# Kernel tuning notes

Measured on AMD Instinct MI355X. Metric: run time of the kernel, lower is better.

Reference implementation:

```python
import jax, jax.numpy as jnp
import numpy as np

VOCAB, EMB, HID, CTXD = 32000, 512, 1024, 2048
B, T, L = 64, 64, 64

def setup_inputs() -> dict:
    key = jax.random.key(0)
    ks = jax.random.split(key, 10)
    return {
        "tgt": jax.random.randint(ks[0], (B, T), 0, VOCAB, dtype=jnp.int64 if jax.config.jax_enable_x64 else jnp.int32),
        "ctx": jax.random.normal(ks[1], (B, L, CTXD), dtype=jnp.float32),
        "h0": jax.random.normal(ks[2], (B, HID), dtype=jnp.float32),
        "ctx_lengths": jax.random.randint(ks[3], (B,), 1, L + 1),
        "emb_table": jax.random.normal(ks[4], (VOCAB, EMB), dtype=jnp.float32) * 0.01,
        "W_a": jax.random.normal(ks[5], (HID, CTXD), dtype=jnp.float32) * 0.01,
        "W_ih": jax.random.normal(ks[6], (3 * HID, EMB + CTXD), dtype=jnp.float32) * 0.01,
        "W_hh": jax.random.normal(ks[7], (3 * HID, HID), dtype=jnp.float32) * 0.01,
        "b_ih": jnp.zeros((3 * HID,), dtype=jnp.float32),
        "b_hh": jnp.zeros((3 * HID,), dtype=jnp.float32),
    }

def reference(tgt, ctx, h0, ctx_lengths, emb_table, W_a, W_ih, W_hh, b_ih, b_hh):
    H = h0.shape[-1]
    Lc = ctx.shape[1]
    # length mask over context positions: [B, L]
    mask = jnp.arange(Lc)[None, :] < ctx_lengths[:, None]
    # precompute 'general' attention projection of ctx: [B, L, H]
    ctxW = jnp.einsum('blc,hc->blh', ctx, W_a)
    emb = emb_table[tgt]  # [B, T, E]

    def step(h, e_t):
        # Bahdanau-style: attend with previous hidden state
        scores = jnp.einsum('bh,blh->bl', h, ctxW)
        scores = jnp.where(mask, scores, jnp.float32(-1e9))
        attn = jax.nn.softmax(scores, axis=-1)
        c_t = jnp.einsum('bl,blc->bc', attn, ctx)  # [B, CTXD]
        x = jnp.concatenate([e_t, c_t], axis=-1)   # [B, E+CTXD]
        gx = x @ W_ih.T + b_ih                      # [B, 3H]
        gh = h @ W_hh.T + b_hh                      # [B, 3H]
        r = jax.nn.sigmoid(gx[:, :H] + gh[:, :H])
        z = jax.nn.sigmoid(gx[:, H:2 * H] + gh[:, H:2 * H])
        n = jnp.tanh(gx[:, 2 * H:] + r * gh[:, 2 * H:])
        h_new = (1.0 - z) * n + z * h
        return h_new, h_new

    h_last, outs = jax.lax.scan(step, h0, jnp.swapaxes(emb, 0, 1))
    return jnp.swapaxes(outs, 0, 1), h_last  # (B, T, H), (B, H)
```

## Files before the change

kernel.cpp:

```cpp
#include <hip/hip_runtime.h>
#include <hip/hip_bf16.h>


using short8 = __attribute__((ext_vector_type(8))) short;
using f32x4  = __attribute__((ext_vector_type(4))) float;

#define FLAG_ACC 1
#define FLAG_BF  2

__device__ __forceinline__ void gld16(const void* g, void* l) {
  __builtin_amdgcn_global_load_lds(
      (const __attribute__((address_space(1))) unsigned int*)g,
      (__attribute__((address_space(3))) unsigned int*)l, 16, 0, 0);
}


__global__ __launch_bounds__(256) void split_bf16_kernel(
    const float* __restrict__ x, __hip_bfloat16* __restrict__ hi,
    __hip_bfloat16* __restrict__ lo, int n)
{
  int i = blockIdx.x * blockDim.x + threadIdx.x;
  int stride = gridDim.x * blockDim.x;
  for (; i < n; i += stride) {
    float v = x[i];
    __hip_bfloat16 h = __float2bfloat16(v);
    hi[i] = h;
    lo[i] = __float2bfloat16(v - __bfloat162float(h));
  }
}

__global__ __launch_bounds__(256) void prep_weights(
    const float* __restrict__ Wih, const float* __restrict__ Whh,
    const float* __restrict__ bih, const float* __restrict__ bhh,
    __hip_bfloat16* __restrict__ WcH, __hip_bfloat16* __restrict__ WcL,
    __hip_bfloat16* __restrict__ We,
    __hip_bfloat16* __restrict__ WhH, __hip_bfloat16* __restrict__ WhL,
    float* __restrict__ bihp, float* __restrict__ bhhp)
{
  const int jp = blockIdx.x;
  const int u = jp / 3, g = jp - 3 * u;
  const int src = g * 1024 + u;
  for (int c = threadIdx.x; c < 2048; c += 256) {
    float v = Wih[(size_t)src * 2560 + 512 + c];
    __hip_bfloat16 h = __float2bfloat16(v);
    WcH[(size_t)jp * 2048 + c] = h;
    WcL[(size_t)jp * 2048 + c] = __float2bfloat16(v - __bfloat162float(h));
  }
  for (int c = threadIdx.x; c < 512; c += 256)
    We[(size_t)jp * 512 + c] = __float2bfloat16(Wih[(size_t)src * 2560 + c]);
  for (int c = threadIdx.x; c < 1024; c += 256) {
    float v = Whh[(size_t)src * 1024 + c];
    __hip_bfloat16 h = __float2bfloat16(v);
    WhH[(size_t)jp * 1024 + c] = h;
    WhL[(size_t)jp * 1024 + c] = __float2bfloat16(v - __bfloat162float(h));
  }
  if (threadIdx.x == 0) { bihp[jp] = bih[src]; bhhp[jp] = bhh[src]; }
}

__global__ __launch_bounds__(256) void emb_gather(
    const int* __restrict__ tgt, const float* __restrict__ table,
    __hip_bfloat16* __restrict__ outb)
{
  const int row = blockIdx.x;
  const int v = tgt[row];
  for (int c = threadIdx.x; c < 512; c += 256)
    outb[(size_t)row * 512 + c] = __float2bfloat16(table[(size_t)v * 512 + c]);
}

__global__ __launch_bounds__(256) void h0_init(
    const float* __restrict__ h0, float* __restrict__ hf,
    __hip_bfloat16* __restrict__ hhi, __hip_bfloat16* __restrict__ hlo)
{
  const int i = blockIdx.x * 256 + threadIdx.x;
  float v = h0[i];
  hf[i] = v;
  __hip_bfloat16 h = __float2bfloat16(v);
  hhi[i] = h;
  hlo[i] = __float2bfloat16(v - __bfloat162float(h));
}


__global__ __launch_bounds__(256) void gemm_bt(
    const short* __restrict__ A, const short* __restrict__ B,
    float* __restrict__ Cf, __hip_bfloat16* __restrict__ Cb,
    const float* __restrict__ bias, int M, int N, int K, int flags)
{
  __shared__ __align__(16) short As[128 * 32];
  __shared__ __align__(16) short Bs[128 * 32];
  const int tid = threadIdx.x, lane = tid & 63, w = tid >> 6;
  const int m0 = blockIdx.y * 128, n0 = blockIdx.x * 128;
  const int wm = (w >> 1) * 64, wn = (w & 1) * 64;
  const int srow = lane >> 2, scol = (lane & 3) * 8;
  f32x4 zero = {0.f, 0.f, 0.f, 0.f};
  f32x4 acc[4][4];
#pragma unroll
  for (int i = 0; i < 4; ++i)
#pragma unroll
    for (int j = 0; j < 4; ++j) acc[i][j] = zero;

  for (int k0 = 0; k0 < K; k0 += 32) {
    __syncthreads();
#pragma unroll
    for (int s = 0; s < 2; ++s) {
      const int chunk = w * 2 + s;
      const int r = chunk * 16 + srow;
      gld16(A + (size_t)(m0 + r) * K + k0 + scol, As + chunk * 512);
      gld16(B + (size_t)(n0 + r) * K + k0 + scol, Bs + chunk * 512);
    }
    __syncthreads();
    const int fm = lane & 15, fq = lane >> 4;
    short8 af[4], bq[4];
#pragma unroll
    for (int i = 0; i < 4; ++i)
      af[i] = *(const short8*)(As + (wm + i * 16 + fm) * 32 + fq * 8);
#pragma unroll
    for (int j = 0; j < 4; ++j)
      bq[j] = *(const short8*)(Bs + (wn + j * 16 + fm) * 32 + fq * 8);
#pragma unroll
    for (int i = 0; i < 4; ++i)
#pragma unroll
      for (int j = 0; j < 4; ++j)
        acc[i][j] = __builtin_amdgcn_mfma_f32_16x16x32_bf16(af[i], bq[j], acc[i][j], 0, 0, 0);
  }

  const int cn = lane & 15, cq = (lane >> 4) * 4;
#pragma unroll
  for (int i = 0; i < 4; ++i)
#pragma unroll
    for (int j = 0; j < 4; ++j)
#pragma unroll
      for (int r = 0; r < 4; ++r) {
        const int m = m0 + wm + i * 16 + cq + r;
        const int n = n0 + wn + j * 16 + cn;
        float v = acc[i][j][r];
        if (flags & FLAG_ACC) v += Cf[(size_t)m * N + n];
        if (bias) v += bias[n];
        if (flags & FLAG_BF) Cb[(size_t)m * N + n] = __float2bfloat16(v);
        else                 Cf[(size_t)m * N + n] = v;
      }
}


__global__ __launch_bounds__(256) void gemm_bt3(
    const short* __restrict__ AH, const short* __restrict__ AL,
    const short* __restrict__ BH, const short* __restrict__ BL,
    float* __restrict__ Cf, int M, int N, int K)
{
  __shared__ __align__(16) short AsH[128 * 32];
  __shared__ __align__(16) short AsL[128 * 32];
  __shared__ __align__(16) short BsH[128 * 32];
  __shared__ __align__(16) short BsL[128 * 32];
  const int tid = threadIdx.x, lane = tid & 63, w = tid >> 6;
  const int m0 = blockIdx.y * 128, n0 = blockIdx.x * 128;
  const int wm = (w >> 1) * 64, wn = (w & 1) * 64;
  const int srow = lane >> 2, scol = (lane & 3) * 8;
  f32x4 zero = {0.f, 0.f, 0.f, 0.f};
  f32x4 acc[4][4];
#pragma unroll
  for (int i = 0; i < 4; ++i)
#pragma unroll
    for (int j = 0; j < 4; ++j) acc[i][j] = zero;

  for (int k0 = 0; k0 < K; k0 += 32) {
    __syncthreads();
#pragma unroll
    for (int s = 0; s < 2; ++s) {
      const int chunk = w * 2 + s;
      const int r = chunk * 16 + srow;
      const size_t ao = (size_t)(m0 + r) * K + k0 + scol;
      const size_t bo = (size_t)(n0 + r) * K + k0 + scol;
      gld16(AH + ao, AsH + chunk * 512);
      gld16(AL + ao, AsL + chunk * 512);
      gld16(BH + bo, BsH + chunk * 512);
      gld16(BL + bo, BsL + chunk * 512);
    }
    __syncthreads();
    const int fm = lane & 15, fq = lane >> 4;
    short8 ah[4], al[4], bh[4], bl[4];
#pragma unroll
    for (int i = 0; i < 4; ++i) {
      const int off = (wm + i * 16 + fm) * 32 + fq * 8;
      ah[i] = *(const short8*)(AsH + off);
      al[i] = *(const short8*)(AsL + off);
    }
#pragma unroll
    for (int j = 0; j < 4; ++j) {
      const int off = (wn + j * 16 + fm) * 32 + fq * 8;
      bh[j] = *(const short8*)(BsH + off);
      bl[j] = *(const short8*)(BsL + off);
    }
#pragma unroll
    for (int i = 0; i < 4; ++i)
#pragma unroll
      for (int j = 0; j < 4; ++j) {
        acc[i][j] = __builtin_amdgcn_mfma_f32_16x16x32_bf16(ah[i], bh[j], acc[i][j], 0, 0, 0);
        acc[i][j] = __builtin_amdgcn_mfma_f32_16x16x32_bf16(al[i], bh[j], acc[i][j], 0, 0, 0);
        acc[i][j] = __builtin_amdgcn_mfma_f32_16x16x32_bf16(ah[i], bl[j], acc[i][j], 0, 0, 0);
      }
  }

  const int cn = lane & 15, cq = (lane >> 4) * 4;
#pragma unroll
  for (int i = 0; i < 4; ++i)
#pragma unroll
    for (int j = 0; j < 4; ++j)
#pragma unroll
      for (int r = 0; r < 4; ++r) {
        const int m = m0 + wm + i * 16 + cq + r;
        const int n = n0 + wn + j * 16 + cn;
        Cf[(size_t)m * N + n] = acc[i][j][r];
      }
}


__global__ __launch_bounds__(256) void step_a(
    const float* __restrict__ hf, const float* __restrict__ ctxW,
    const int* __restrict__ lens, float* __restrict__ attn,
    const short* __restrict__ hhi, const short* __restrict__ hlo,
    const short* __restrict__ WhH, const short* __restrict__ WhL,
    float* __restrict__ ghG)
{
  const int tid = threadIdx.x;
  if (blockIdx.x < 64) {
    __shared__ float hs[1024];
    __shared__ float part[256];
    const int b = blockIdx.x;
    const int len = lens[b];
    ((float4*)hs)[tid] = ((const float4*)(hf + b * 1024))[tid];
    __syncthreads();
    const int l = tid >> 2, q = tid & 3;
    float sx = 0.f, sy = 0.f, sz = 0.f, sw = 0.f;
    if (l < len) {
      const float4* row = (const float4*)(ctxW + ((size_t)(b * 64 + l)) * 1024 + q * 256);
      const float4* hh = (const float4*)(hs + q * 256);
#pragma unroll 8
      for (int i = 0; i < 64; ++i) {
        float4 a = row[i], c = hh[i];
        sx += a.x * c.x; sy += a.y * c.y; sz += a.z * c.z; sw += a.w * c.w;
      }
    }
    part[tid] = (sx + sy) + (sz + sw);
    __syncthreads();
    if (tid < 64) {
      float sc = part[tid * 4] + part[tid * 4 + 1] + part[tid * 4 + 2] + part[tid * 4 + 3];
      if (tid >= len) sc = -1e9f;
      float m = sc;
#pragma unroll
      for (int off = 32; off > 0; off >>= 1) m = fmaxf(m, __shfl_xor(m, off));
      float e = __expf(sc - m);
      float sum = e;
#pragma unroll
      for (int off = 32; off > 0; off >>= 1) sum += __shfl_xor(sum, off);
      attn[b * 64 + tid] = e / sum;
    }
  } else {
    const int j0 = (blockIdx.x - 64) * 16;
    const int lane = tid & 63, w = tid >> 6;
    const int fm = lane & 15, fq = lane >> 4;
    f32x4 acc = {0.f, 0.f, 0.f, 0.f};
    const short* ah = hhi + (w * 16 + fm) * 1024 + fq * 8;
    const short* al = hlo + (w * 16 + fm) * 1024 + fq * 8;
    const short* bh = WhH + (size_t)(j0 + fm) * 1024 + fq * 8;
    const short* bl = WhL + (size_t)(j0 + fm) * 1024 + fq * 8;
#pragma unroll 4
    for (int k0 = 0; k0 < 1024; k0 += 32) {
      short8 aH = *(const short8*)(ah + k0);
      short8 aL = *(const short8*)(al + k0);
      short8 b0 = *(const short8*)(bh + k0);
      short8 c0 = *(const short8*)(bl + k0);
      acc = __builtin_amdgcn_mfma_f32_16x16x32_bf16(aH, b0, acc, 0, 0, 0);
      acc = __builtin_amdgcn_mfma_f32_16x16x32_bf16(aL, b0, acc, 0, 0, 0);
      acc = __builtin_amdgcn_mfma_f32_16x16x32_bf16(aH, c0, acc, 0, 0, 0);
    }
    const int mb = w * 16 + fq * 4;
    *(f32x4*)(ghG + (size_t)(j0 + fm) * 64 + mb) = acc;
  }
}


__global__ __launch_bounds__(512) void gate_kernel(
    const float* __restrict__ attn, const int* __restrict__ lens,
    const float* __restrict__ ghG, const float* __restrict__ ctxWc,
    const __hip_bfloat16* __restrict__ gxe, const float* __restrict__ bhhp,
    float* __restrict__ hf, short* __restrict__ hhi, short* __restrict__ hlo,
    float* __restrict__ out, int t)
{
  const int jc = blockIdx.x & 63, bc = blockIdx.x >> 6;
  const int j0 = jc * 48, b0 = bc * 16;
  __shared__ float ghs[48 * 17];
  __shared__ float wv[16][64];
  __shared__ short lidx[16][64];
  __shared__ int   cnt[16];
  __shared__ float ps0[256], ps1[256], ps2[256];
  const int tid = threadIdx.x;
  if (tid < 16) cnt[tid] = 0;
  for (int i = tid; i < 768; i += 512) {
    const int row = i >> 4, col = i & 15;
    ghs[row * 17 + col] = ghG[(size_t)(j0 + row) * 64 + b0 + col];
  }
  __syncthreads();
  if (tid < 256) {
    const int bb = tid >> 4, l4 = (tid & 15) * 4;
    const int b = b0 + bb, len = lens[b];
#pragma unroll
    for (int k = 0; k < 4; ++k) {
      const int l = l4 + k;
      const float wl = attn[b * 64 + l];
      if (l < len && wl >= 1e-8f) {
        const int pos = atomicAdd(&cnt[bb], 1);
        lidx[bb][pos] = (short)l;
        wv[bb][pos] = wl;
      }
    }
  }
  __syncthreads();

  const int tl = tid & 255;
  const int bb = tl >> 4, jg = tl & 15;
  const int b = b0 + bb;
  const int n = cnt[bb];
  const int nh = n >> 1;
  const int ibeg = (tid < 256) ? 0 : nh;
  const int iend = (tid < 256) ? nh : n;
  float g0 = 0.f, g1 = 0.f, g2 = 0.f;
  const float* base = ctxWc + (size_t)(b * 64) * 3072 + j0 + jg * 3;
  int i = ibeg;
  for (; i + 3 < iend; i += 4) {
    const float w0 = wv[bb][i],     w1 = wv[bb][i + 1];
    const float w2 = wv[bb][i + 2], w3 = wv[bb][i + 3];
    const float* p0 = base + (size_t)lidx[bb][i] * 3072;
    const float* p1 = base + (size_t)lidx[bb][i + 1] * 3072;
    const float* p2 = base + (size_t)lidx[bb][i + 2] * 3072;
    const float* p3 = base + (size_t)lidx[bb][i + 3] * 3072;
    const float a0 = __builtin_nontemporal_load(p0);
    const float a1 = __builtin_nontemporal_load(p0 + 1);
    const float a2 = __builtin_nontemporal_load(p0 + 2);
    const float b0v = __builtin_nontemporal_load(p1);
    const float b1v = __builtin_nontemporal_load(p1 + 1);
    const float b2v = __builtin_nontemporal_load(p1 + 2);
    const float c0 = __builtin_nontemporal_load(p2);
    const float c1 = __builtin_nontemporal_load(p2 + 1);
    const float c2 = __builtin_nontemporal_load(p2 + 2);
    const float d0 = __builtin_nontemporal_load(p3);
    const float d1 = __builtin_nontemporal_load(p3 + 1);
    const float d2 = __builtin_nontemporal_load(p3 + 2);
    g0 += (w0 * a0 + w1 * b0v) + (w2 * c0 + w3 * d0);
    g1 += (w0 * a1 + w1 * b1v) + (w2 * c1 + w3 * d1);
    g2 += (w0 * a2 + w1 * b2v) + (w2 * c2 + w3 * d2);
  }
  for (; i < iend; ++i) {
    const float wa = wv[bb][i];
    const float* pa = base + (size_t)lidx[bb][i] * 3072;
    g0 += wa * __builtin_nontemporal_load(pa);
    g1 += wa * __builtin_nontemporal_load(pa + 1);
    g2 += wa * __builtin_nontemporal_load(pa + 2);
  }
  if (tid >= 256) { ps0[tl] = g0; ps1[tl] = g1; ps2[tl] = g2; }
  __syncthreads();
  if (tid < 256) {
    g0 += ps0[tl]; g1 += ps1[tl]; g2 += ps2[tl];

    const int jp = j0 + jg * 3;
    const __hip_bfloat16* ge = gxe + (size_t)(b * 64 + t) * 3072 + jp;
    const float gxr = g0 + __bfloat162float(ge[0]);
    const float gxz = g1 + __bfloat162float(ge[1]);
    const float gxn = g2 + __bfloat162float(ge[2]);
    const float ghr = ghs[(jg * 3 + 0) * 17 + bb] + bhhp[jp + 0];
    const float ghz = ghs[(jg * 3 + 1) * 17 + bb] + bhhp[jp + 1];
    const float ghn = ghs[(jg * 3 + 2) * 17 + bb] + bhhp[jp + 2];
    const float rr = 1.f / (1.f + __expf(-(gxr + ghr)));
    const float zz = 1.f / (1.f + __expf(-(gxz + ghz)));
    const float nn = tanhf(gxn + rr * ghn);
    const int u = jc * 16 + jg;
    const float hold = hf[b * 1024 + u];
    const float hn = (1.f - zz) * nn + zz * hold;
    out[(size_t)(b * 64 + t) * 1024 + u] = hn;
    hf[b * 1024 + u] = hn;
    __hip_bfloat16 hh = __float2bfloat16(hn);
    hhi[b * 1024 + u] = *reinterpret_cast<short*>(&hh);
    __hip_bfloat16 hl = __float2bfloat16(hn - __bfloat162float(hh));
    hlo[b * 1024 + u] = *reinterpret_cast<short*>(&hl);
    if (t == 63) out[(size_t)64 * 64 * 1024 + b * 1024 + u] = hn;
  }
}


extern "C" void kernel_launch(void* const* d_in, const int* in_sizes, int n_in,
                              void* d_out, int out_size, void* d_ws, size_t ws_size,
                              hipStream_t stream)
{
  const int*   tgt  = (const int*)  d_in[0];
  const float* ctx  = (const float*)d_in[1];
  const float* h0   = (const float*)d_in[2];
  const int*   lens = (const int*)  d_in[3];
  const float* embt = (const float*)d_in[4];
  const float* Wa   = (const float*)d_in[5];
  const float* Wih  = (const float*)d_in[6];
  const float* Whh  = (const float*)d_in[7];
  const float* bih  = (const float*)d_in[8];
  const float* bhh  = (const float*)d_in[9];
  float* out = (float*)d_out;

  char* p = (char*)d_ws;
  auto take = [&](size_t bytes) {
    char* q = p;
    p += (bytes + 255) & ~(size_t)255;
    return q;
  };
  short* ctx_hi = (short*)take((size_t)8388608 * 2);
  short* ctx_lo = (short*)take((size_t)8388608 * 2);
  short* Wa_hi  = (short*)take((size_t)2097152 * 2);
  short* Wa_lo  = (short*)take((size_t)2097152 * 2);
  short* WcH    = (short*)take((size_t)3072 * 2048 * 2);
  short* WcL    = (short*)take((size_t)3072 * 2048 * 2);
  short* We_p   = (short*)take((size_t)3072 * 512 * 2);
  short* WhH    = (short*)take((size_t)3072 * 1024 * 2);
  short* WhL    = (short*)take((size_t)3072 * 1024 * 2);
  float* bih_p  = (float*)take(3072 * 4);
  float* bhh_p  = (float*)take(3072 * 4);
  short* emb_bf = (short*)take((size_t)4096 * 512 * 2);
  float* ctxW   = (float*)take((size_t)4096 * 1024 * 4);
  float* ctxWc  = (float*)take((size_t)4096 * 3072 * 4);
  short* gxe    = (short*)take((size_t)4096 * 3072 * 2);
  float* hf     = (float*)take((size_t)65536 * 4);
  short* hhi    = (short*)take((size_t)65536 * 2);
  short* hlo    = (short*)take((size_t)65536 * 2);
  float* attn   = (float*)take((size_t)4096 * 4);
  float* ghG    = (float*)take((size_t)3072 * 64 * 4);

  split_bf16_kernel<<<2048, 256, 0, stream>>>(ctx, (__hip_bfloat16*)ctx_hi,
                                              (__hip_bfloat16*)ctx_lo, 8388608);
  split_bf16_kernel<<<1024, 256, 0, stream>>>(Wa, (__hip_bfloat16*)Wa_hi,
                                              (__hip_bfloat16*)Wa_lo, 2097152);
  prep_weights<<<3072, 256, 0, stream>>>(Wih, Whh, bih, bhh,
      (__hip_bfloat16*)WcH, (__hip_bfloat16*)WcL, (__hip_bfloat16*)We_p,
      (__hip_bfloat16*)WhH, (__hip_bfloat16*)WhL, bih_p, bhh_p);
  emb_gather<<<4096, 256, 0, stream>>>(tgt, embt, (__hip_bfloat16*)emb_bf);
  h0_init<<<256, 256, 0, stream>>>(h0, hf, (__hip_bfloat16*)hhi,
                                   (__hip_bfloat16*)hlo);

  gemm_bt3<<<dim3(8, 32), 256, 0, stream>>>(ctx_hi, ctx_lo, Wa_hi, Wa_lo,
                                            ctxW, 4096, 1024, 2048);
  gemm_bt3<<<dim3(24, 32), 256, 0, stream>>>(ctx_hi, ctx_lo, WcH, WcL,
                                             ctxWc, 4096, 3072, 2048);
  gemm_bt<<<dim3(24, 32), 256, 0, stream>>>(emb_bf, We_p, nullptr,
                                            (__hip_bfloat16*)gxe, bih_p,
                                            4096, 3072, 512, FLAG_BF);

  for (int t = 0; t < 64; ++t) {
    step_a<<<256, 256, 0, stream>>>(hf, ctxW, lens, attn,
                                    hhi, hlo, WhH, WhL, ghG);
    gate_kernel<<<256, 512, 0, stream>>>(attn, lens, ghG, ctxWc,
        (const __hip_bfloat16*)gxe, bhh_p, hf, hhi, hlo, out, t);
  }
}
```

Before: 2.414 ms.

## Fuse per-step recurrence kernels into one persistent cooperative kernel with grid barriers

Replaces the 128 per-timestep launches (step_a and gate_kernel) with a single cooperative persistent kernel of 256 blocks. The blocks synchronise through atomic counter barriers in global memory, and each block reloads h and converts it to hi/lo bf16 in LDS. The Whh GEMM is also split across two K-halves per block, with the halves reduced in shared memory. This targets launch overhead on the serial recurrence, but adds spin-wait barrier cost and relies on relaxed atomics to make writes visible across blocks.

```diff
diff --git a/kernel.cpp b/kernel.cpp
--- a/kernel.cpp
+++ b/kernel.cpp
@@ -7,6 +7,9 @@
 
 #define FLAG_ACC 1
 #define FLAG_BF  2
+
+#define AL(p)    __hip_atomic_load((p), __ATOMIC_RELAXED, __HIP_MEMORY_SCOPE_AGENT)
+#define AS(p, v) __hip_atomic_store((p), (v), __ATOMIC_RELAXED, __HIP_MEMORY_SCOPE_AGENT)
 
 __device__ __forceinline__ void gld16(const void* g, void* l) {
   __builtin_amdgcn_global_load_lds(
@@ -69,14 +72,11 @@
 
 __global__ __launch_bounds__(256) void h0_init(
     const float* __restrict__ h0, float* __restrict__ hf,
-    __hip_bfloat16* __restrict__ hhi, __hip_bfloat16* __restrict__ hlo)
+    unsigned int* __restrict__ bar)
 {
   const int i = blockIdx.x * 256 + threadIdx.x;
-  float v = h0[i];
-  hf[i] = v;
-  __hip_bfloat16 h = __float2bfloat16(v);
-  hhi[i] = h;
-  hlo[i] = __float2bfloat16(v - __bfloat162float(h));
+  hf[i] = h0[i];
+  if (blockIdx.x == 0 && threadIdx.x < 256) bar[threadIdx.x] = 0u;
 }
 
 
@@ -213,174 +213,215 @@
 }
 
 
-__global__ __launch_bounds__(256) void step_a(
-    const float* __restrict__ hf, const float* __restrict__ ctxW,
-    const int* __restrict__ lens, float* __restrict__ attn,
-    const short* __restrict__ hhi, const short* __restrict__ hlo,
+__global__ __launch_bounds__(512, 1) void recurrence_kernel(
+    const float* __restrict__ ctxW, const int* __restrict__ lens,
     const short* __restrict__ WhH, const short* __restrict__ WhL,
-    float* __restrict__ ghG)
-{
+    const float* __restrict__ ctxWc, const __hip_bfloat16* __restrict__ gxe,
+    const float* __restrict__ bhhp, float* __restrict__ hf,
+    float* __restrict__ attn, float* __restrict__ ghG,
+    unsigned int* __restrict__ bar, float* __restrict__ out)
+{
+  const int blk = blockIdx.x;
   const int tid = threadIdx.x;
-  if (blockIdx.x < 64) {
-    __shared__ float hs[1024];
-    __shared__ float part[256];
-    const int b = blockIdx.x;
-    const int len = lens[b];
-    ((float4*)hs)[tid] = ((const float4*)(hf + b * 1024))[tid];
-    __syncthreads();
-    const int l = tid >> 2, q = tid & 3;
-    float sx = 0.f, sy = 0.f, sz = 0.f, sw = 0.f;
-    if (l < len) {
-      const float4* row = (const float4*)(ctxW + ((size_t)(b * 64 + l)) * 1024 + q * 256);
-      const float4* hh = (const float4*)(hs + q * 256);
-#pragma unroll 8
-      for (int i = 0; i < 64; ++i) {
-        float4 a = row[i], c = hh[i];
-        sx += a.x * c.x; sy += a.y * c.y; sz += a.z * c.z; sw += a.w * c.w;
-      }
-    }
-    part[tid] = (sx + sy) + (sz + sw);
-    __syncthreads();
-    if (tid < 64) {
-      float sc = part[tid * 4] + part[tid * 4 + 1] + part[tid * 4 + 2] + part[tid * 4 + 3];
-      if (tid >= len) sc = -1e9f;
-      float m = sc;
-#pragma unroll
-      for (int off = 32; off > 0; off >>= 1) m = fmaxf(m, __shfl_xor(m, off));
-      float e = __expf(sc - m);
-      float sum = e;
-#pragma unroll
-      for (int off = 32; off > 0; off >>= 1) sum += __shfl_xor(sum, off);
-      attn[b * 64 + tid] = e / sum;
-    }
-  } else {
-    const int j0 = (blockIdx.x - 64) * 16;
-    const int lane = tid & 63, w = tid >> 6;
-    const int fm = lane & 15, fq = lane >> 4;
-    f32x4 acc = {0.f, 0.f, 0.f, 0.f};
-    const short* ah = hhi + (w * 16 + fm) * 1024 + fq * 8;
-    const short* al = hlo + (w * 16 + fm) * 1024 + fq * 8;
-    const short* bh = WhH + (size_t)(j0 + fm) * 1024 + fq * 8;
-    const short* bl = WhL + (size_t)(j0 + fm) * 1024 + fq * 8;
-#pragma unroll 4
-    for (int k0 = 0; k0 < 1024; k0 += 32) {
-      short8 aH = *(const short8*)(ah + k0);
-      short8 aL = *(const short8*)(al + k0);
-      short8 b0 = *(const short8*)(bh + k0);
-      short8 c0 = *(const short8*)(bl + k0);
-      acc = __builtin_amdgcn_mfma_f32_16x16x32_bf16(aH, b0, acc, 0, 0, 0);
-      acc = __builtin_amdgcn_mfma_f32_16x16x32_bf16(aL, b0, acc, 0, 0, 0);
-      acc = __builtin_amdgcn_mfma_f32_16x16x32_bf16(aH, c0, acc, 0, 0, 0);
-    }
-    const int mb = w * 16 + fq * 4;
-    *(f32x4*)(ghG + (size_t)(j0 + fm) * 64 + mb) = acc;
-  }
-}
-
-
-__global__ __launch_bounds__(512) void gate_kernel(
-    const float* __restrict__ attn, const int* __restrict__ lens,
-    const float* __restrict__ ghG, const float* __restrict__ ctxWc,
-    const __hip_bfloat16* __restrict__ gxe, const float* __restrict__ bhhp,
-    float* __restrict__ hf, short* __restrict__ hhi, short* __restrict__ hlo,
-    float* __restrict__ out, int t)
-{
-  const int jc = blockIdx.x & 63, bc = blockIdx.x >> 6;
-  const int j0 = jc * 48, b0 = bc * 16;
+
+  __shared__ float hs[1024];
+  __shared__ float part[256];
+  __shared__ __align__(16) short AsH[16 * 1032];
+  __shared__ __align__(16) short AsL[16 * 1032];
+  __shared__ f32x4 psk[4][64];
   __shared__ float ghs[48 * 17];
   __shared__ float wv[16][64];
   __shared__ short lidx[16][64];
   __shared__ int   cnt[16];
   __shared__ float ps0[256], ps1[256], ps2[256];
-  const int tid = threadIdx.x;
-  if (tid < 16) cnt[tid] = 0;
-  for (int i = tid; i < 768; i += 512) {
-    const int row = i >> 4, col = i & 15;
-    ghs[row * 17 + col] = ghG[(size_t)(j0 + row) * 64 + b0 + col];
-  }
-  __syncthreads();
-  if (tid < 256) {
-    const int bb = tid >> 4, l4 = (tid & 15) * 4;
-    const int b = b0 + bb, len = lens[b];
-#pragma unroll
-    for (int k = 0; k < 4; ++k) {
-      const int l = l4 + k;
-      const float wl = attn[b * 64 + l];
-      if (l < len && wl >= 1e-8f) {
-        const int pos = atomicAdd(&cnt[bb], 1);
-        lidx[bb][pos] = (short)l;
-        wv[bb][pos] = wl;
-      }
-    }
-  }
-  __syncthreads();
-
-  const int tl = tid & 255;
-  const int bb = tl >> 4, jg = tl & 15;
-  const int b = b0 + bb;
-  const int n = cnt[bb];
-  const int nh = n >> 1;
-  const int ibeg = (tid < 256) ? 0 : nh;
-  const int iend = (tid < 256) ? nh : n;
-  float g0 = 0.f, g1 = 0.f, g2 = 0.f;
-  const float* base = ctxWc + (size_t)(b * 64) * 3072 + j0 + jg * 3;
-  int i = ibeg;
-  for (; i + 3 < iend; i += 4) {
-    const float w0 = wv[bb][i],     w1 = wv[bb][i + 1];
-    const float w2 = wv[bb][i + 2], w3 = wv[bb][i + 3];
-    const float* p0 = base + (size_t)lidx[bb][i] * 3072;
-    const float* p1 = base + (size_t)lidx[bb][i + 1] * 3072;
-    const float* p2 = base + (size_t)lidx[bb][i + 2] * 3072;
-    const float* p3 = base + (size_t)lidx[bb][i + 3] * 3072;
-    const float a0 = __builtin_nontemporal_load(p0);
-    const float a1 = __builtin_nontemporal_load(p0 + 1);
-    const float a2 = __builtin_nontemporal_load(p0 + 2);
-    const float b0v = __builtin_nontemporal_load(p1);
-    const float b1v = __builtin_nontemporal_load(p1 + 1);
-    const float b2v = __builtin_nontemporal_load(p1 + 2);
-    const float c0 = __builtin_nontemporal_load(p2);
-    const float c1 = __builtin_nontemporal_load(p2 + 1);
-    const float c2 = __builtin_nontemporal_load(p2 + 2);
-    const float d0 = __builtin_nontemporal_load(p3);
-    const float d1 = __builtin_nontemporal_load(p3 + 1);
-    const float d2 = __builtin_nontemporal_load(p3 + 2);
-    g0 += (w0 * a0 + w1 * b0v) + (w2 * c0 + w3 * d0);
-    g1 += (w0 * a1 + w1 * b1v) + (w2 * c1 + w3 * d1);
-    g2 += (w0 * a2 + w1 * b2v) + (w2 * c2 + w3 * d2);
-  }
-  for (; i < iend; ++i) {
-    const float wa = wv[bb][i];
-    const float* pa = base + (size_t)lidx[bb][i] * 3072;
-    g0 += wa * __builtin_nontemporal_load(pa);
-    g1 += wa * __builtin_nontemporal_load(pa + 1);
-    g2 += wa * __builtin_nontemporal_load(pa + 2);
-  }
-  if (tid >= 256) { ps0[tl] = g0; ps1[tl] = g1; ps2[tl] = g2; }
-  __syncthreads();
-  if (tid < 256) {
-    g0 += ps0[tl]; g1 += ps1[tl]; g2 += ps2[tl];
-
-    const int jp = j0 + jg * 3;
-    const __hip_bfloat16* ge = gxe + (size_t)(b * 64 + t) * 3072 + jp;
-    const float gxr = g0 + __bfloat162float(ge[0]);
-    const float gxz = g1 + __bfloat162float(ge[1]);
-    const float gxn = g2 + __bfloat162float(ge[2]);
-    const float ghr = ghs[(jg * 3 + 0) * 17 + bb] + bhhp[jp + 0];
-    const float ghz = ghs[(jg * 3 + 1) * 17 + bb] + bhhp[jp + 1];
-    const float ghn = ghs[(jg * 3 + 2) * 17 + bb] + bhhp[jp + 2];
-    const float rr = 1.f / (1.f + __expf(-(gxr + ghr)));
-    const float zz = 1.f / (1.f + __expf(-(gxz + ghz)));
-    const float nn = tanhf(gxn + rr * ghn);
-    const int u = jc * 16 + jg;
-    const float hold = hf[b * 1024 + u];
-    const float hn = (1.f - zz) * nn + zz * hold;
-    out[(size_t)(b * 64 + t) * 1024 + u] = hn;
-    hf[b * 1024 + u] = hn;
-    __hip_bfloat16 hh = __float2bfloat16(hn);
-    hhi[b * 1024 + u] = *reinterpret_cast<short*>(&hh);
-    __hip_bfloat16 hl = __float2bfloat16(hn - __bfloat162float(hh));
-    hlo[b * 1024 + u] = *reinterpret_cast<short*>(&hl);
-    if (t == 63) out[(size_t)64 * 64 * 1024 + b * 1024 + u] = hn;
+
+  const int g = blk - 64;
+  const int xcd = g & 7, s = g >> 3;
+  const int jc2 = xcd * 6 + (s >> 2);
+  const int bc2 = s & 3;
+
+  for (int t = 0; t < 64; ++t) {
+    if (blk < 64) {
+      const int b = blk;
+      const int len = lens[b];
+      for (int i = tid; i < 1024; i += 512)
+        hs[i] = AL(hf + b * 1024 + i);
+      __syncthreads();
+      if (tid < 256) {
+        const int l = tid >> 2, q = tid & 3;
+        float sx = 0.f, sy = 0.f, sz = 0.f, sw = 0.f;
+        if (l < len) {
+          const float4* row = (const float4*)(ctxW + ((size_t)(b * 64 + l)) * 1024 + q * 256);
+          const float4* hh = (const float4*)(hs + q * 256);
+#pragma unroll 8
+          for (int i = 0; i < 64; ++i) {
+            float4 a = row[i], c = hh[i];
+            sx += a.x * c.x; sy += a.y * c.y; sz += a.z * c.z; sw += a.w * c.w;
+          }
+        }
+        part[tid] = (sx + sy) + (sz + sw);
+      }
+      __syncthreads();
+      if (tid < 64) {
+        float sc = part[tid * 4] + part[tid * 4 + 1] + part[tid * 4 + 2] + part[tid * 4 + 3];
+        if (tid >= len) sc = -1e9f;
+        float m = sc;
+#pragma unroll
+        for (int off = 32; off > 0; off >>= 1) m = fmaxf(m, __shfl_xor(m, off));
+        float e = __expf(sc - m);
+        float sum = e;
+#pragma unroll
+        for (int off = 32; off > 0; off >>= 1) sum += __shfl_xor(sum, off);
+        AS(attn + b * 64 + tid, e / sum);
+      }
+    } else {
+      for (int i = tid; i < 16384; i += 512) {
+        const int row = i >> 10, col = i & 1023;
+        float v = AL(hf + (bc2 * 16 + row) * 1024 + col);
+        __hip_bfloat16 hh = __float2bfloat16(v);
+        AsH[row * 1032 + col] = *reinterpret_cast<short*>(&hh);
+        __hip_bfloat16 hl = __float2bfloat16(v - __bfloat162float(hh));
+        AsL[row * 1032 + col] = *reinterpret_cast<short*>(&hl);
+      }
+      __syncthreads();
+      const int lane = tid & 63, w = tid >> 6;
+      const int fm = lane & 15, fq = lane >> 4;
+      const int jsub = w & 3, khalf = w >> 2;
+      const int jr = jc2 * 64 + jsub * 16 + fm;
+      const short* bh = WhH + (size_t)jr * 1024 + fq * 8;
+      const short* bl = WhL + (size_t)jr * 1024 + fq * 8;
+      const short* arH = AsH + fm * 1032 + fq * 8;
+      const short* arL = AsL + fm * 1032 + fq * 8;
+      f32x4 acc = {0.f, 0.f, 0.f, 0.f};
+      const int kbeg = khalf * 512;
+#pragma unroll 4
+      for (int k = kbeg; k < kbeg + 512; k += 32) {
+        short8 aH = *(const short8*)(arH + k);
+        short8 aL = *(const short8*)(arL + k);
+        short8 b0 = *(const short8*)(bh + k);
+        short8 c0 = *(const short8*)(bl + k);
+        acc = __builtin_amdgcn_mfma_f32_16x16x32_bf16(aH, b0, acc, 0, 0, 0);
+        acc = __builtin_amdgcn_mfma_f32_16x16x32_bf16(aL, b0, acc, 0, 0, 0);
+        acc = __builtin_amdgcn_mfma_f32_16x16x32_bf16(aH, c0, acc, 0, 0, 0);
+      }
+      if (khalf) psk[jsub][lane] = acc;
+      __syncthreads();
+      if (!khalf) {
+        f32x4 o = psk[jsub][lane];
+        acc.x += o.x; acc.y += o.y; acc.z += o.z; acc.w += o.w;
+        const size_t bidx = (size_t)jr * 64 + bc2 * 16 + fq * 4;
+        AS(ghG + bidx + 0, acc.x);
+        AS(ghG + bidx + 1, acc.y);
+        AS(ghG + bidx + 2, acc.z);
+        AS(ghG + bidx + 3, acc.w);
+      }
+    }
+
+    __syncthreads();
+    if (tid == 0) {
+      __hip_atomic_fetch_add(&bar[t * 2], 1u, __ATOMIC_RELAXED, __HIP_MEMORY_SCOPE_AGENT);
+      while (AL(&bar[t * 2]) < 256u) __builtin_amdgcn_s_sleep(2);
+    }
+    __syncthreads();
+
+    {
+      const int jc = blk & 63, bc = blk >> 6;
+      const int j0 = jc * 48, b0 = bc * 16;
+      if (tid < 16) cnt[tid] = 0;
+      for (int i = tid; i < 768; i += 512) {
+        const int row = i >> 4, col = i & 15;
+        ghs[row * 17 + col] = AL(ghG + (size_t)(j0 + row) * 64 + b0 + col);
+      }
+      __syncthreads();
+      if (tid < 256) {
+        const int bb = tid >> 4, l4 = (tid & 15) * 4;
+        const int b = b0 + bb, len = lens[b];
+#pragma unroll
+        for (int k = 0; k < 4; ++k) {
+          const int l = l4 + k;
+          const float wl = AL(attn + b * 64 + l);
+          if (l < len && wl >= 1e-8f) {
+            const int pos = atomicAdd(&cnt[bb], 1);
+            lidx[bb][pos] = (short)l;
+            wv[bb][pos] = wl;
+          }
+        }
+      }
+      __syncthreads();
+
+      const int tl = tid & 255;
+      const int bb = tl >> 4, jg = tl & 15;
+      const int b = b0 + bb;
+      const int n = cnt[bb];
+      const int nh = n >> 1;
+      const int ibeg = (tid < 256) ? 0 : nh;
+      const int iend = (tid < 256) ? nh : n;
+      float g0 = 0.f, g1 = 0.f, g2 = 0.f;
+      const float* base = ctxWc + (size_t)(b * 64) * 3072 + j0 + jg * 3;
+      int i = ibeg;
+      for (; i + 3 < iend; i += 4) {
+        const float w0 = wv[bb][i],     w1 = wv[bb][i + 1];
+        const float w2 = wv[bb][i + 2], w3 = wv[bb][i + 3];
+        const float* p0 = base + (size_t)lidx[bb][i] * 3072;
+        const float* p1 = base + (size_t)lidx[bb][i + 1] * 3072;
+        const float* p2 = base + (size_t)lidx[bb][i + 2] * 3072;
+        const float* p3 = base + (size_t)lidx[bb][i + 3] * 3072;
+        const float a0 = __builtin_nontemporal_load(p0);
+        const float a1 = __builtin_nontemporal_load(p0 + 1);
+        const float a2 = __builtin_nontemporal_load(p0 + 2);
+        const float b0v = __builtin_nontemporal_load(p1);
+        const float b1v = __builtin_nontemporal_load(p1 + 1);
+        const float b2v = __builtin_nontemporal_load(p1 + 2);
+        const float c0 = __builtin_nontemporal_load(p2);
+        const float c1 = __builtin_nontemporal_load(p2 + 1);
+        const float c2 = __builtin_nontemporal_load(p2 + 2);
+        const float d0 = __builtin_nontemporal_load(p3);
+        const float d1 = __builtin_nontemporal_load(p3 + 1);
+        const float d2 = __builtin_nontemporal_load(p3 + 2);
+        g0 += (w0 * a0 + w1 * b0v) + (w2 * c0 + w3 * d0);
+        g1 += (w0 * a1 + w1 * b1v) + (w2 * c1 + w3 * d1);
+        g2 += (w0 * a2 + w1 * b2v) + (w2 * c2 + w3 * d2);
+      }
+      for (; i < iend; ++i) {
+        const float wa = wv[bb][i];
+        const float* pa = base + (size_t)lidx[bb][i] * 3072;
+        g0 += wa * __builtin_nontemporal_load(pa);
+        g1 += wa * __builtin_nontemporal_load(pa + 1);
+        g2 += wa * __builtin_nontemporal_load(pa + 2);
+      }
+      if (tid >= 256) { ps0[tl] = g0; ps1[tl] = g1; ps2[tl] = g2; }
+      __syncthreads();
+      if (tid < 256) {
+        g0 += ps0[tl]; g1 += ps1[tl]; g2 += ps2[tl];
+
+        const int jp = j0 + jg * 3;
+        const __hip_bfloat16* ge = gxe + (size_t)(b * 64 + t) * 3072 + jp;
+        const float gxr = g0 + __bfloat162float(ge[0]);
+        const float gxz = g1 + __bfloat162float(ge[1]);
+        const float gxn = g2 + __bfloat162float(ge[2]);
+        const float ghr = ghs[(jg * 3 + 0) * 17 + bb] + bhhp[jp + 0];
+        const float ghz = ghs[(jg * 3 + 1) * 17 + bb] + bhhp[jp + 1];
+        const float ghn = ghs[(jg * 3 + 2) * 17 + bb] + bhhp[jp + 2];
+        const float rr = 1.f / (1.f + __expf(-(gxr + ghr)));
+        const float zz = 1.f / (1.f + __expf(-(gxz + ghz)));
+        const float nn = tanhf(gxn + rr * ghn);
+        const int u = jc * 16 + jg;
+        const float hold = AL(hf + b * 1024 + u);
+        const float hn = (1.f - zz) * nn + zz * hold;
+        out[(size_t)(b * 64 + t) * 1024 + u] = hn;
+        AS(hf + b * 1024 + u, hn);
+        if (t == 63) out[(size_t)64 * 64 * 1024 + b * 1024 + u] = hn;
+      }
+    }
+
+    if (t != 63) {
+      __syncthreads();
+      if (tid == 0) {
+        __hip_atomic_fetch_add(&bar[t * 2 + 1], 1u, __ATOMIC_RELAXED, __HIP_MEMORY_SCOPE_AGENT);
+        while (AL(&bar[t * 2 + 1]) < 256u) __builtin_amdgcn_s_sleep(2);
+      }
+      __syncthreads();
+    }
   }
 }
 
@@ -423,10 +464,9 @@
   float* ctxWc  = (float*)take((size_t)4096 * 3072 * 4);
   short* gxe    = (short*)take((size_t)4096 * 3072 * 2);
   float* hf     = (float*)take((size_t)65536 * 4);
-  short* hhi    = (short*)take((size_t)65536 * 2);
-  short* hlo    = (short*)take((size_t)65536 * 2);
   float* attn   = (float*)take((size_t)4096 * 4);
   float* ghG    = (float*)take((size_t)3072 * 64 * 4);
+  unsigned int* bar = (unsigned int*)take(256 * 4);
 
   split_bf16_kernel<<<2048, 256, 0, stream>>>(ctx, (__hip_bfloat16*)ctx_hi,
                                               (__hip_bfloat16*)ctx_lo, 8388608);
@@ -436,8 +476,7 @@
       (__hip_bfloat16*)WcH, (__hip_bfloat16*)WcL, (__hip_bfloat16*)We_p,
       (__hip_bfloat16*)WhH, (__hip_bfloat16*)WhL, bih_p, bhh_p);
   emb_gather<<<4096, 256, 0, stream>>>(tgt, embt, (__hip_bfloat16*)emb_bf);
-  h0_init<<<256, 256, 0, stream>>>(h0, hf, (__hip_bfloat16*)hhi,
-                                   (__hip_bfloat16*)hlo);
+  h0_init<<<256, 256, 0, stream>>>(h0, hf, bar);
 
   gemm_bt3<<<dim3(8, 32), 256, 0, stream>>>(ctx_hi, ctx_lo, Wa_hi, Wa_lo,
                                             ctxW, 4096, 1024, 2048);
@@ -447,10 +486,17 @@
                                             (__hip_bfloat16*)gxe, bih_p,
                                             4096, 3072, 512, FLAG_BF);
 
-  for (int t = 0; t < 64; ++t) {
-    step_a<<<256, 256, 0, stream>>>(hf, ctxW, lens, attn,
-                                    hhi, hlo, WhH, WhL, ghG);
-    gate_kernel<<<256, 512, 0, stream>>>(attn, lens, ghG, ctxWc,
-        (const __hip_bfloat16*)gxe, bhh_p, hf, hhi, hlo, out, t);
-  }
-}
+  {
+    const float* ctxWb = ctxW; const float* ctxWcB = ctxWc;
+    const short* WhHc = WhH;  const short* WhLc = WhL;
+    const __hip_bfloat16* gxeB = (const __hip_bfloat16*)gxe;
+    const float* bhhB = bhh_p;
+    void* kargs[] = {
+      (void*)&ctxWb, (void*)&lens, (void*)&WhHc, (void*)&WhLc,
+      (void*)&ctxWcB, (void*)&gxeB, (void*)&bhhB,
+      (void*)&hf, (void*)&attn, (void*)&ghG, (void*)&bar, (void*)&out
+    };
+    hipLaunchCooperativeKernel((void*)recurrence_kernel, dim3(256), dim3(512),
+                               kargs, 0, stream);
+  }
+}
```

Result: slower. 3.500 ms (+45.0%).

## Swizzle GEMM LDS layout and split gate kernel across more blocks

Applied to the files above, without the earlier changes.

Applies an XOR swizzle to the LDS column offsets in both bf16 GEMM kernels, on the global-to-LDS store side and the fragment read side, to cut bank conflicts during fragment loads. The per-step gate kernel now handles 8 batch rows per block instead of 16 and launches 512 blocks. Each block splits the attention-weighted ctxWc gather four ways across thread quarters instead of two, with a three-way partial-sum reduction. The gate change aims to raise parallelism and memory-level concurrency in the latency-bound recurrent loop, at the cost of more blocks and extra shared-memory reduction work.

```diff
diff --git a/kernel.cpp b/kernel.cpp
--- a/kernel.cpp
+++ b/kernel.cpp
@@ -90,7 +90,8 @@
   const int tid = threadIdx.x, lane = tid & 63, w = tid >> 6;
   const int m0 = blockIdx.y * 128, n0 = blockIdx.x * 128;
   const int wm = (w >> 1) * 64, wn = (w & 1) * 64;
-  const int srow = lane >> 2, scol = (lane & 3) * 8;
+  const int srow = lane >> 2;
+  const int scol = (((lane & 3) ^ ((lane >> 3) & 3)) * 8);
   f32x4 zero = {0.f, 0.f, 0.f, 0.f};
   f32x4 acc[4][4];
 #pragma unroll
@@ -109,13 +110,14 @@
     }
     __syncthreads();
     const int fm = lane & 15, fq = lane >> 4;
+    const int cbs = (fq ^ ((fm >> 1) & 3)) * 8;
     short8 af[4], bq[4];
 #pragma unroll
     for (int i = 0; i < 4; ++i)
-      af[i] = *(const short8*)(As + (wm + i * 16 + fm) * 32 + fq * 8);
+      af[i] = *(const short8*)(As + (wm + i * 16 + fm) * 32 + cbs);
 #pragma unroll
     for (int j = 0; j < 4; ++j)
-      bq[j] = *(const short8*)(Bs + (wn + j * 16 + fm) * 32 + fq * 8);
+      bq[j] = *(const short8*)(Bs + (wn + j * 16 + fm) * 32 + cbs);
 #pragma unroll
     for (int i = 0; i < 4; ++i)
 #pragma unroll
@@ -153,7 +155,8 @@
   const int tid = threadIdx.x, lane = tid & 63, w = tid >> 6;
   const int m0 = blockIdx.y * 128, n0 = blockIdx.x * 128;
   const int wm = (w >> 1) * 64, wn = (w & 1) * 64;
-  const int srow = lane >> 2, scol = (lane & 3) * 8;
+  const int srow = lane >> 2;
+  const int scol = (((lane & 3) ^ ((lane >> 3) & 3)) * 8);
   f32x4 zero = {0.f, 0.f, 0.f, 0.f};
   f32x4 acc[4][4];
 #pragma unroll
@@ -176,16 +179,17 @@
     }
     __syncthreads();
     const int fm = lane & 15, fq = lane >> 4;
+    const int cbs = (fq ^ ((fm >> 1) & 3)) * 8;
     short8 ah[4], al[4], bh[4], bl[4];
 #pragma unroll
     for (int i = 0; i < 4; ++i) {
-      const int off = (wm + i * 16 + fm) * 32 + fq * 8;
+      const int off = (wm + i * 16 + fm) * 32 + cbs;
       ah[i] = *(const short8*)(AsH + off);
       al[i] = *(const short8*)(AsL + off);
     }
 #pragma unroll
     for (int j = 0; j < 4; ++j) {
-      const int off = (wn + j * 16 + fm) * 32 + fq * 8;
+      const int off = (wn + j * 16 + fm) * 32 + cbs;
       bh[j] = *(const short8*)(BsH + off);
       bl[j] = *(const short8*)(BsL + off);
     }
@@ -286,20 +290,20 @@
     float* __restrict__ out, int t)
 {
   const int jc = blockIdx.x & 63, bc = blockIdx.x >> 6;
-  const int j0 = jc * 48, b0 = bc * 16;
-  __shared__ float ghs[48 * 17];
-  __shared__ float wv[16][64];
-  __shared__ short lidx[16][64];
-  __shared__ int   cnt[16];
-  __shared__ float ps0[256], ps1[256], ps2[256];
+  const int j0 = jc * 48, b0 = bc * 8;
+  __shared__ float ghs[48 * 9];
+  __shared__ float wv[8][64];
+  __shared__ short lidx[8][64];
+  __shared__ int   cnt[8];
+  __shared__ float ps0[384], ps1[384], ps2[384];
   const int tid = threadIdx.x;
-  if (tid < 16) cnt[tid] = 0;
-  for (int i = tid; i < 768; i += 512) {
-    const int row = i >> 4, col = i & 15;
-    ghs[row * 17 + col] = ghG[(size_t)(j0 + row) * 64 + b0 + col];
+  if (tid < 8) cnt[tid] = 0;
+  if (tid < 384) {
+    const int row = tid >> 3, col = tid & 7;
+    ghs[row * 9 + col] = ghG[(size_t)(j0 + row) * 64 + b0 + col];
   }
   __syncthreads();
-  if (tid < 256) {
+  if (tid < 128) {
     const int bb = tid >> 4, l4 = (tid & 15) * 4;
     const int b = b0 + bb, len = lens[b];
 #pragma unroll
@@ -315,13 +319,12 @@
   }
   __syncthreads();
 
-  const int tl = tid & 255;
+  const int q = tid >> 7, tl = tid & 127;
   const int bb = tl >> 4, jg = tl & 15;
   const int b = b0 + bb;
   const int n = cnt[bb];
-  const int nh = n >> 1;
-  const int ibeg = (tid < 256) ? 0 : nh;
-  const int iend = (tid < 256) ? nh : n;
+  const int ibeg = (q * n) >> 2;
+  const int iend = ((q + 1) * n) >> 2;
   float g0 = 0.f, g1 = 0.f, g2 = 0.f;
   const float* base = ctxWc + (size_t)(b * 64) * 3072 + j0 + jg * 3;
   int i = ibeg;
@@ -355,19 +358,24 @@
     g1 += wa * __builtin_nontemporal_load(pa + 1);
     g2 += wa * __builtin_nontemporal_load(pa + 2);
   }
-  if (tid >= 256) { ps0[tl] = g0; ps1[tl] = g1; ps2[tl] = g2; }
+  if (q) {
+    const int o = (q - 1) * 128 + tl;
+    ps0[o] = g0; ps1[o] = g1; ps2[o] = g2;
+  }
   __syncthreads();
-  if (tid < 256) {
-    g0 += ps0[tl]; g1 += ps1[tl]; g2 += ps2[tl];
+  if (q == 0) {
+    g0 += (ps0[tl] + ps0[128 + tl]) + ps0[256 + tl];
+    g1 += (ps1[tl] + ps1[128 + tl]) + ps1[256 + tl];
+    g2 += (ps2[tl] + ps2[128 + tl]) + ps2[256 + tl];
 
     const int jp = j0 + jg * 3;
     const __hip_bfloat16* ge = gxe + (size_t)(b * 64 + t) * 3072 + jp;
     const float gxr = g0 + __bfloat162float(ge[0]);
     const float gxz = g1 + __bfloat162float(ge[1]);
     const float gxn = g2 + __bfloat162float(ge[2]);
-    const float ghr = ghs[(jg * 3 + 0) * 17 + bb] + bhhp[jp + 0];
-    const float ghz = ghs[(jg * 3 + 1) * 17 + bb] + bhhp[jp + 1];
-    const float ghn = ghs[(jg * 3 + 2) * 17 + bb] + bhhp[jp + 2];
+    const float ghr = ghs[(jg * 3 + 0) * 9 + bb] + bhhp[jp + 0];
+    const float ghz = ghs[(jg * 3 + 1) * 9 + bb] + bhhp[jp + 1];
+    const float ghn = ghs[(jg * 3 + 2) * 9 + bb] + bhhp[jp + 2];
     const float rr = 1.f / (1.f + __expf(-(gxr + ghr)));
     const float zz = 1.f / (1.f + __expf(-(gxz + ghz)));
     const float nn = tanhf(gxn + rr * ghn);
@@ -450,7 +458,7 @@
   for (int t = 0; t < 64; ++t) {
     step_a<<<256, 256, 0, stream>>>(hf, ctxW, lens, attn,
                                     hhi, hlo, WhH, WhL, ghG);
-    gate_kernel<<<256, 512, 0, stream>>>(attn, lens, ghG, ctxWc,
+    gate_kernel<<<512, 512, 0, stream>>>(attn, lens, ghG, ctxWc,
         (const __hip_bfloat16*)gxe, bhh_p, hf, hhi, hlo, out, t);
   }
 }
```

Result: faster. 2.284 ms (-5.4%).
